# Kernel tuning notes

Hardware: AMD Instinct MI355X
Metric: run time of the kernel (lower is better)

The kernel has to match this reference:

```python
import jax, jax.numpy as jnp
import numpy as np

R = 32  # voxel resolution

def leaky(x):
    return jnp.where(x > 0, x, 0.1 * x)

def bn(x, gamma, beta, axes, eps=1e-4):
    mu = jnp.mean(x, axis=axes, keepdims=True)
    var = jnp.var(x, axis=axes, keepdims=True)
    shape = [1] * x.ndim
    shape[1] = x.shape[1]
    g = gamma.reshape(shape)
    b = beta.reshape(shape)
    return (x - mu) * jax.lax.rsqrt(var + eps) * g + b

def voxelize(features, coords, r):
    # features: (B, C, N), coords: (B, 3, N)
    B, C, N = features.shape
    mean = jnp.mean(coords, axis=2, keepdims=True)
    norm = (coords - mean + 1.0) / 2.0 * r
    norm = jnp.clip(norm, 0.0, r - 1.0)            # (B, 3, N) continuous voxel coords
    vox = jnp.round(norm).astype(jnp.int32)
    flat = (vox[:, 0] * r + vox[:, 1]) * r + vox[:, 2]      # (B, N)
    seg = (flat + jnp.arange(B, dtype=jnp.int32)[:, None] * (r ** 3)).reshape(-1)
    data = features.transpose(0, 2, 1).reshape(B * N, C)
    sums = jax.ops.segment_sum(data, seg, num_segments=B * r ** 3)
    cnt = jax.ops.segment_sum(jnp.ones((B * N,), data.dtype), seg, num_segments=B * r ** 3)
    avg = sums / jnp.maximum(cnt, 1.0)[:, None]
    grid = avg.reshape(B, r, r, r, C).transpose(0, 4, 1, 2, 3)  # (B, C, r, r, r)
    return grid, norm

def trilinear_devoxelize(grid, norm, r):
    # grid: (B, C, r, r, r), norm: (B, 3, N) in [0, r-1]
    B, C = grid.shape[:2]
    N = norm.shape[2]
    lo = jnp.floor(norm).astype(jnp.int32)
    frac = norm - lo.astype(norm.dtype)
    hi = jnp.minimum(lo + 1, r - 1)
    gf = grid.reshape(B, C, r ** 3)
    out = jnp.zeros((B, C, N), grid.dtype)
    for dx in (0, 1):
        for dy in (0, 1):
            for dz in (0, 1):
                ix = hi[:, 0] if dx else lo[:, 0]
                iy = hi[:, 1] if dy else lo[:, 1]
                iz = hi[:, 2] if dz else lo[:, 2]
                wx = frac[:, 0] if dx else 1.0 - frac[:, 0]
                wy = frac[:, 1] if dy else 1.0 - frac[:, 1]
                wz = frac[:, 2] if dz else 1.0 - frac[:, 2]
                idx = (ix * r + iy) * r + iz                    # (B, N)
                g = jnp.take_along_axis(gf, idx[:, None, :], axis=2)  # (B, C, N)
                out = out + g * (wx * wy * wz)[:, None, :]
    return out

def conv3d(x, w, b):
    y = jax.lax.conv_general_dilated(
        x, w, window_strides=(1, 1, 1), padding=[(1, 1)] * 3,
        dimension_numbers=('NCDHW', 'OIDHW', 'NCDHW'))
    return y + b[None, :, None, None, None]

def setup_inputs() -> dict:
    key = jax.random.key(0)
    ks = jax.random.split(key, 8)
    B, Cin, Cout, N = 8, 64, 64, 32768
    s1 = 1.0 / np.sqrt(Cin * 27)
    s2 = 1.0 / np.sqrt(Cout * 27)
    return {
        'features': jax.random.normal(ks[0], (B, Cin, N), jnp.float32),
        'coords': jax.random.normal(ks[1], (B, 3, N), jnp.float32),
        'conv1_w': jax.random.normal(ks[2], (Cout, Cin, 3, 3, 3), jnp.float32) * s1,
        'conv1_b': jnp.zeros((Cout,), jnp.float32),
        'bn1_g': jnp.ones((Cout,), jnp.float32),
        'bn1_b': jnp.zeros((Cout,), jnp.float32),
        'conv2_w': jax.random.normal(ks[3], (Cout, Cout, 3, 3, 3), jnp.float32) * s2,
        'conv2_b': jnp.zeros((Cout,), jnp.float32),
        'bn2_g': jnp.ones((Cout,), jnp.float32),
        'bn2_b': jnp.zeros((Cout,), jnp.float32),
        'mlp_w': jax.random.normal(ks[4], (Cout, Cin), jnp.float32) / np.sqrt(Cin),
        'mlp_b': jnp.zeros((Cout,), jnp.float32),
        'bnp_g': jnp.ones((Cout,), jnp.float32),
        'bnp_b': jnp.zeros((Cout,), jnp.float32),
    }

def reference(features, coords, conv1_w, conv1_b, bn1_g, bn1_b,
              conv2_w, conv2_b, bn2_g, bn2_b, mlp_w, mlp_b, bnp_g, bnp_b):
    grid, norm = voxelize(features, coords, R)
    v = leaky(bn(conv3d(grid, conv1_w, conv1_b), bn1_g, bn1_b, (0, 2, 3, 4)))
    v = leaky(bn(conv3d(v, conv2_w, conv2_b), bn2_g, bn2_b, (0, 2, 3, 4)))
    sampled = trilinear_devoxelize(v, norm, R)                 # (B, Cout, N)
    p = jnp.einsum('oi,bin->bon', mlp_w, features) + mlp_b[None, :, None]
    p = leaky(bn(p, bnp_g, bnp_b, (0, 2)))
    fused = sampled + p
    return fused, v
```

## Files before the change

kernel.cpp:

```cpp
#include <hip/hip_runtime.h>
#include <hip/hip_bf16.h>

#define BB 8
#define CC 64
#define NPTS 32768
#define RR 32
#define RV 32768
#define MTOT (BB*RV)
#define EPSV 1e-4f

#define OFF_BUFA 0u
#define OFF_BUFB 16777216u
#define OFF_WB1  25165824u
#define OFF_WB2  25221120u
#define OFF_ZG   25276416u
#define OFF_BASE 25276480u
#define OFF_AUX  25800768u
#define OFF_CELL 25801024u
#define OFF_CNT  26063168u
#define OFF_MEAN 26325312u
#define OFF_PART1 26325504u
#define OFF_PART2 26456576u
#define OFF_SCL1 26587648u
#define OFF_SFT1 26587712u
#define OFF_SCL2 26587776u
#define OFF_SFT2 26587840u
#define OFF_WM   26587904u
#define OFF_PARTP 26590208u
#define OFF_SCLP 27114496u
#define OFF_SFTP 27114560u
#define OFF_NORM 33554432u

typedef __attribute__((ext_vector_type(8))) __bf16 bf16x8;
typedef __attribute__((ext_vector_type(8))) unsigned short u16x8;
typedef __attribute__((ext_vector_type(4))) float f32x4;

__device__ __forceinline__ float b2f(ushort u) {
    union { unsigned u; float f; } x; x.u = ((unsigned)u) << 16; return x.f;
}
__device__ __forceinline__ ushort f2b(float f) {
    __hip_bfloat16 h = __float2bfloat16(f);
    return *reinterpret_cast<ushort*>(&h);
}

__global__ void k_coord_mean(const float* __restrict__ coords, float* __restrict__ mean) {
    int ba = blockIdx.x >> 3, ch = blockIdx.x & 7;
    const float* src = coords + (size_t)ba * NPTS + ch * 4096;
    float s = 0.f;
    for (int i = threadIdx.x; i < 4096; i += 256) s += src[i];
    __shared__ float red[256];
    red[threadIdx.x] = s; __syncthreads();
    for (int w = 128; w > 0; w >>= 1) {
        if (threadIdx.x < w) red[threadIdx.x] += red[threadIdx.x + w];
        __syncthreads();
    }
    if (threadIdx.x == 0) atomicAdd(&mean[ba], red[0]);
}

__global__ void k_cellid(const float* __restrict__ coords, const float* __restrict__ mean,
                         float* __restrict__ norm, int* __restrict__ cellid,
                         unsigned* __restrict__ cnt) {
    int idx = blockIdx.x * 256 + threadIdx.x;
    int b = idx >> 15, n = idx & (NPTS - 1);
    int flat = 0;
    #pragma unroll
    for (int a = 0; a < 3; ++a) {
        float c = coords[((size_t)(b * 3 + a)) * NPTS + n];
        float nm = (c - mean[b * 3 + a] * (1.0f / NPTS) + 1.0f) * (0.5f * RR);
        nm = fminf(fmaxf(nm, 0.0f), (float)(RR - 1));
        norm[((size_t)(b * 3 + a)) * NPTS + n] = nm;
        flat = flat * RR + (int)rintf(nm);
    }
    int cell = b * RV + flat;
    cellid[idx] = cell;
    atomicAdd(&cnt[cell], 1u);
}

__global__ void k_scan1(const unsigned* __restrict__ cnt, unsigned* __restrict__ base,
                        unsigned* __restrict__ aux) {
    int tid = threadIdx.x;
    int c0 = blockIdx.x * 1024 + tid * 4;
    unsigned v0 = cnt[c0], v1 = cnt[c0 + 1], v2 = cnt[c0 + 2], v3 = cnt[c0 + 3];
    unsigned tot = v0 + v1 + v2 + v3;
    __shared__ unsigned sc[256];
    sc[tid] = tot; __syncthreads();
    for (int off = 1; off < 256; off <<= 1) {
        unsigned t = (tid >= off) ? sc[tid - off] : 0u;
        __syncthreads();
        sc[tid] += t;
        __syncthreads();
    }
    unsigned excl = sc[tid] - tot;
    base[c0] = excl;
    base[c0 + 1] = excl + v0;
    base[c0 + 2] = excl + v0 + v1;
    base[c0 + 3] = excl + v0 + v1 + v2;
    if (tid == 255) aux[blockIdx.x] = sc[255];
}

__global__ void k_scan2(unsigned* __restrict__ aux) {
    int tid = threadIdx.x;
    unsigned own = aux[tid];
    __shared__ unsigned sc[256];
    sc[tid] = own; __syncthreads();
    for (int off = 1; off < 256; off <<= 1) {
        unsigned t = (tid >= off) ? sc[tid - off] : 0u;
        __syncthreads();
        sc[tid] += t;
        __syncthreads();
    }
    aux[tid] = sc[tid] - own;
}

__global__ void k_scan3(unsigned* __restrict__ base, const unsigned* __restrict__ aux) {
    int i = blockIdx.x * 256 + threadIdx.x;
    base[i] += aux[i >> 10];
}

__global__ __launch_bounds__(256) void k_scatfeat(
    const float* __restrict__ feats, const int* __restrict__ cellid,
    unsigned* __restrict__ base, ushort* __restrict__ fsort,
    const ushort* __restrict__ wmb, const float* __restrict__ mbias,
    ushort* __restrict__ pb, float* __restrict__ partp) {
    __shared__ float t[64 * 65];
    __shared__ unsigned spos[64];
    __shared__ float sf[512];
    int b = blockIdx.x >> 9;
    int n0 = (blockIdx.x & 511) * 64;
    int tid = threadIdx.x;
    #pragma unroll
    for (int k = 0; k < 16; ++k) {
        int idx = k * 256 + tid;
        int c = idx >> 6, nl = idx & 63;
        t[c * 65 + nl] = feats[((size_t)(b * 64 + c)) * NPTS + n0 + nl];
    }
    if (tid < 64) {
        int cell = cellid[(b << 15) + n0 + tid];
        spos[tid] = atomicAdd(&base[cell], 1u);
    }
    __syncthreads();
    #pragma unroll
    for (int it = 0; it < 2; ++it) {
        int pl = it * 32 + (tid >> 3);
        int j = tid & 7;
        unsigned pos = spos[pl];
        u16x8 v;
        #pragma unroll
        for (int k = 0; k < 8; ++k) v[k] = f2b(t[(j * 8 + k) * 65 + pl]);
        *reinterpret_cast<u16x8*>(fsort + (((size_t)pos) << 6) + j * 8) = v;
    }
    int w = tid >> 6, l = tid & 63;
    int nl = l & 15, kg = l >> 4;
    bf16x8 Af[2];
    #pragma unroll
    for (int ks = 0; ks < 2; ++ks) {
        union { u16x8 u; bf16x8 h; } cv;
        #pragma unroll
        for (int j = 0; j < 8; ++j)
            cv.u[j] = f2b(t[(ks * 32 + kg * 8 + j) * 65 + w * 16 + nl]);
        Af[ks] = cv.h;
    }
    f32x4 acc[4];
    #pragma unroll
    for (int cb = 0; cb < 4; ++cb) acc[cb] = (f32x4){0.f, 0.f, 0.f, 0.f};
    #pragma unroll
    for (int ks = 0; ks < 2; ++ks)
        #pragma unroll
        for (int cb = 0; cb < 4; ++cb) {
            bf16x8 Bf = *reinterpret_cast<const bf16x8*>(wmb + (cb * 16 + nl) * 64 + ks * 32 + kg * 8);
            acc[cb] = __builtin_amdgcn_mfma_f32_16x16x32_bf16(Af[ks], Bf, acc[cb], 0, 0, 0);
        }
    float ss[4] = {0.f, 0.f, 0.f, 0.f}, qq[4] = {0.f, 0.f, 0.f, 0.f};
    #pragma unroll
    for (int cb = 0; cb < 4; ++cb) {
        float bsv = mbias[cb * 16 + nl];
        #pragma unroll
        for (int r = 0; r < 4; ++r) {
            float yv = acc[cb][r] + bsv;
            int pt = w * 16 + kg * 4 + r;
            pb[(((size_t)((b << 15) + n0 + pt)) << 6) + cb * 16 + nl] = f2b(yv);
            ss[cb] += yv; qq[cb] += yv * yv;
        }
    }
    #pragma unroll
    for (int cb = 0; cb < 4; ++cb) {
        ss[cb] += __shfl_xor(ss[cb], 16); ss[cb] += __shfl_xor(ss[cb], 32);
        qq[cb] += __shfl_xor(qq[cb], 16); qq[cb] += __shfl_xor(qq[cb], 32);
    }
    if (l < 16) {
        #pragma unroll
        for (int cb = 0; cb < 4; ++cb) {
            sf[w * 128 + cb * 16 + nl] = ss[cb];
            sf[w * 128 + 64 + cb * 16 + nl] = qq[cb];
        }
    }
    __syncthreads();
    if (tid < 128)
        partp[(size_t)tid * 4096 + blockIdx.x] =
            sf[tid] + sf[128 + tid] + sf[256 + tid] + sf[384 + tid];
}

__global__ __launch_bounds__(256) void k_gather(
    const ushort* __restrict__ fsort, const unsigned* __restrict__ base,
    const unsigned* __restrict__ cnt, __hip_bfloat16* __restrict__ xb) {
    int cell = blockIdx.x * 4 + (threadIdx.x >> 6);
    int lane = threadIdx.x & 63;
    unsigned n = cnt[cell];
    unsigned start = base[cell] - n;
    const ushort* rows = fsort + (((size_t)start) << 6) + lane;
    float acc = 0.f;
    unsigned i = 0;
    for (; i + 8 <= n; i += 8) {
        float f0 = b2f(rows[((size_t)(i + 0)) << 6]);
        float f1 = b2f(rows[((size_t)(i + 1)) << 6]);
        float f2 = b2f(rows[((size_t)(i + 2)) << 6]);
        float f3 = b2f(rows[((size_t)(i + 3)) << 6]);
        float f4 = b2f(rows[((size_t)(i + 4)) << 6]);
        float f5 = b2f(rows[((size_t)(i + 5)) << 6]);
        float f6 = b2f(rows[((size_t)(i + 6)) << 6]);
        float f7 = b2f(rows[((size_t)(i + 7)) << 6]);
        acc += ((f0 + f1) + (f2 + f3)) + ((f4 + f5) + (f6 + f7));
    }
    for (; i < n; ++i) acc += b2f(rows[((size_t)i) << 6]);
    float inv = (n > 0) ? (1.0f / (float)n) : 0.f;
    xb[((size_t)cell << 6) + lane] = __float2bfloat16(acc * inv);
}

__global__ void k_wb(const float* __restrict__ w, __hip_bfloat16* __restrict__ wb) {
    int i = blockIdx.x * 256 + threadIdx.x;
    if (i >= CC * CC * 27) return;
    int tap = i % 27, t = i / 27;
    int ci = t & 63, co = t >> 6;
    wb[((size_t)(tap * 64 + co)) * 64 + ci] = __float2bfloat16(w[i]);
}

__global__ void k_wm(const float* __restrict__ w, ushort* __restrict__ wmb) {
    int i = blockIdx.x * 256 + threadIdx.x;
    if (i < 4096) wmb[i] = f2b(w[i]);
}

__global__ void k_act(const ushort* __restrict__ in, const float* __restrict__ scl,
                      const float* __restrict__ sft, ushort* __restrict__ out) {
    size_t i = ((size_t)blockIdx.x * 256 + threadIdx.x) << 3;
    u16x8 v = *reinterpret_cast<const u16x8*>(in + i);
    int c0 = (int)(i & 63);
    u16x8 o;
    #pragma unroll
    for (int j = 0; j < 8; ++j) {
        float f = fmaf(b2f(v[j]), scl[c0 + j], sft[c0 + j]);
        f = f > 0.f ? f : 0.1f * f;
        o[j] = f2b(f);
    }
    *reinterpret_cast<u16x8*>(out + i) = o;
}

__global__ __launch_bounds__(256, 1) void k_conv_mfma(
    const ushort* __restrict__ src, const ushort* __restrict__ wb,
    const float* __restrict__ bias, ushort* __restrict__ y,
    float* __restrict__ part, const ushort* __restrict__ zg) {
    __shared__ __align__(16) char sh[77824 + 49152];
    char* wsh = sh + 77824;
    int tid = threadIdx.x;
    int lane = tid & 63, wid = tid >> 6;
    int tile = ((blockIdx.x & 7) << 7) + (blockIdx.x >> 3);
    int twi = tile & 3, thi = (tile >> 2) & 3;
    int tdi = (tile >> 4) & 7, b = tile >> 7;
    int d0 = tdi * 4, h0 = thi * 8, w0 = twi * 8;

    auto stage_wgt = [&](int g) {
        const ushort* wgrp = wb + g * 12288;
        char* wdst0 = wsh + (g & 1) * 24576;
        #pragma unroll
        for (int i = 0; i < 6; ++i) {
            int c = (i * 4 + wid) * 64 + lane;
            int row = c >> 3, off = c & 7;
            const ushort* gsrc = wgrp + (((row << 3) + (off ^ (row & 7))) << 3);
            char* ldst = wdst0 + ((i * 4 + wid) << 10);
            __builtin_amdgcn_global_load_lds(
                (const __attribute__((address_space(1))) void*)gsrc,
                (__attribute__((address_space(3))) void*)ldst, 16, 0, 0);
        }
    };

    #pragma unroll
    for (int it = 0; it < 19; ++it) {
        int c = (it * 4 + wid) * 64 + lane;
        int row = c >> 3, off = c & 7;
        int dz = row / 100, rem = row - dz * 100;
        int hz = rem / 10, wz = rem - hz * 10;
        int gd = d0 - 1 + dz, gh = h0 - 1 + hz, gw = w0 - 1 + wz;
        int srcoff = off ^ (row & 7);
        const ushort* gsrc = ((unsigned)gd < 32u && (unsigned)gh < 32u && (unsigned)gw < 32u)
            ? src + ((((size_t)((b << 15) | (gd << 10) | (gh << 5) | gw)) << 6) + srcoff * 8)
            : zg;
        char* ldst = sh + ((it * 4 + wid) << 10);
        __builtin_amdgcn_global_load_lds(
            (const __attribute__((address_space(1))) void*)gsrc,
            (__attribute__((address_space(3))) void*)ldst, 16, 0, 0);
    }
    stage_wgt(0);

    int nl = lane & 15, kg = lane >> 4;
    int rbase = wid * 100 + (nl >> 3) * 10 + (nl & 7);
    int bswz = (nl & 7) << 4;

    f32x4 acc[4][4];
    #pragma unroll
    for (int mi = 0; mi < 4; ++mi)
        #pragma unroll
        for (int cb = 0; cb < 4; ++cb) acc[mi][cb] = (f32x4){0.f, 0.f, 0.f, 0.f};

    __syncthreads();

    #pragma unroll 1
    for (int g = 0; g < 9; ++g) {
        if (g < 8) stage_wgt(g + 1);
        const char* wlds = wsh + (g & 1) * 24576;
        int kd = g / 3, kh = g - kd * 3;
        int rr0 = rbase + kd * 100 + kh * 10;
        #pragma unroll
        for (int tl = 0; tl < 3; ++tl) {
            bf16x8 a[4][2];
            #pragma unroll
            for (int mi = 0; mi < 4; ++mi) {
                int r = rr0 + tl + mi * 20;
                int ba = ((r << 7) + (kg << 4)) ^ ((r & 7) << 4);
                a[mi][0] = *reinterpret_cast<const bf16x8*>(sh + ba);
                a[mi][1] = *reinterpret_cast<const bf16x8*>(sh + (ba ^ 64));
            }
            bf16x8 bf[4][2];
            #pragma unroll
            for (int cb = 0; cb < 4; ++cb) {
                int rowb = tl * 64 + cb * 16 + nl;
                int bb0 = ((rowb << 7) + (kg << 4)) ^ bswz;
                bf[cb][0] = *reinterpret_cast<const bf16x8*>(wlds + bb0);
                bf[cb][1] = *reinterpret_cast<const bf16x8*>(wlds + (bb0 ^ 64));
            }
            #pragma unroll
            for (int ks = 0; ks < 2; ++ks)
                #pragma unroll
                for (int mi = 0; mi < 4; ++mi)
                    #pragma unroll
                    for (int cb = 0; cb < 4; ++cb)
                        acc[mi][cb] = __builtin_amdgcn_mfma_f32_16x16x32_bf16(
                            a[mi][ks], bf[cb][ks], acc[mi][cb], 0, 0, 0);
        }
        __syncthreads();
    }

    int d = d0 + wid;
    float bs[4];
    #pragma unroll
    for (int cb = 0; cb < 4; ++cb) bs[cb] = bias[cb * 16 + nl];
    float ss[4] = {0.f, 0.f, 0.f, 0.f}, qq[4] = {0.f, 0.f, 0.f, 0.f};
    #pragma unroll
    for (int mi = 0; mi < 4; ++mi) {
        int h = h0 + mi * 2 + (kg >> 1);
        int w = w0 + (kg & 1) * 4;
        size_t vox = (size_t)((b << 15) | (d << 10) | (h << 5) | w);
        #pragma unroll
        for (int cb = 0; cb < 4; ++cb) {
            int co = cb * 16 + nl;
            #pragma unroll
            for (int r = 0; r < 4; ++r) {
                float yv = acc[mi][cb][r] + bs[cb];
                y[((vox + r) << 6) + co] = f2b(yv);
                ss[cb] += yv; qq[cb] += yv * yv;
            }
        }
    }
    #pragma unroll
    for (int cb = 0; cb < 4; ++cb) {
        ss[cb] += __shfl_xor(ss[cb], 16); ss[cb] += __shfl_xor(ss[cb], 32);
        qq[cb] += __shfl_xor(qq[cb], 16); qq[cb] += __shfl_xor(qq[cb], 32);
    }
    float* sf = (float*)sh;
    if (lane < 16) {
        #pragma unroll
        for (int cb = 0; cb < 4; ++cb) {
            sf[wid * 128 + cb * 16 + nl] = ss[cb];
            sf[wid * 128 + 64 + cb * 16 + nl] = qq[cb];
        }
    }
    __syncthreads();
    if (tid < 128) {
        float t = sf[tid] + sf[128 + tid] + sf[256 + tid] + sf[384 + tid];
        part[tid * 1024 + blockIdx.x] = t;
    }
}

__global__ void k_redbn(const float* __restrict__ part, const float* __restrict__ g,
                        const float* __restrict__ bb, float* __restrict__ scl,
                        float* __restrict__ sft, int cnt) {
    int c = blockIdx.x;
    float s = 0.f, q = 0.f;
    for (int i = threadIdx.x; i < cnt; i += 256) {
        s += part[(size_t)c * cnt + i];
        q += part[(size_t)(64 + c) * cnt + i];
    }
    __shared__ float rs[256], rq[256];
    rs[threadIdx.x] = s; rq[threadIdx.x] = q; __syncthreads();
    for (int w = 128; w > 0; w >>= 1) {
        if (threadIdx.x < w) { rs[threadIdx.x] += rs[threadIdx.x + w]; rq[threadIdx.x] += rq[threadIdx.x + w]; }
        __syncthreads();
    }
    if (threadIdx.x == 0) {
        float mu = rs[0] * (1.0f / MTOT);
        float var = rq[0] * (1.0f / MTOT) - mu * mu;
        float sc = g[c] * rsqrtf(var + EPSV);
        scl[c] = sc; sft[c] = bb[c] - mu * sc;
    }
}

__global__ void k_transpose(const ushort* __restrict__ in, const float* __restrict__ scl,
                            const float* __restrict__ sft, float* __restrict__ out) {
    __shared__ float t[64 * 65];
    size_t base = (size_t)blockIdx.x * 4096;
    int gv0 = blockIdx.x * 64;
    int b = gv0 >> 15;
    int vox0 = gv0 & 32767;
    int chl = threadIdx.x & 63;
    float sc = scl[chl], sf = sft[chl];
    #pragma unroll
    for (int k = 0; k < 16; ++k) {
        int idx = k * 256 + threadIdx.x;
        float v = fmaf(b2f(in[base + idx]), sc, sf);
        t[(idx >> 6) * 65 + (idx & 63)] = v > 0.f ? v : 0.1f * v;
    }
    __syncthreads();
    #pragma unroll
    for (int k = 0; k < 16; ++k) {
        int idx = k * 256 + threadIdx.x;
        int ch = idx >> 6, voxl = idx & 63;
        out[((size_t)(b * 64 + ch)) * RV + vox0 + voxl] = t[voxl * 65 + ch];
    }
}

__global__ __launch_bounds__(256) void k_final(
    float* __restrict__ out, const ushort* __restrict__ pbuf,
    const ushort* __restrict__ vraw, const float* __restrict__ norm,
    const float* __restrict__ scl, const float* __restrict__ sft,
    const float* __restrict__ sclp, const float* __restrict__ sftp) {
    __shared__ float smp[64 * 65];
    int b = blockIdx.x >> 9;
    int n0 = (blockIdx.x & 511) * 64;
    int wid = threadIdx.x >> 6, lane = threadIdx.x & 63;
    const ushort* gb = vraw + (((size_t)b) << 15) * CC;
    const float* nrm0 = norm + ((size_t)(b * 3)) * NPTS;
    float sc = scl[lane], sf = sft[lane];
    float scp = sclp[lane], sfp = sftp[lane];

    #pragma unroll 2
    for (int i = 0; i < 16; ++i) {
        int pl = wid * 16 + i;
        int n = n0 + pl;
        float v0 = nrm0[n];
        float v1 = nrm0[NPTS + n];
        float v2 = nrm0[2 * NPTS + n];
        int lx = (int)floorf(v0), ly = (int)floorf(v1), lz = (int)floorf(v2);
        float fx = v0 - (float)lx, fy = v1 - (float)ly, fz = v2 - (float)lz;
        int hx = min(lx + 1, 31), hy = min(ly + 1, 31), hz = min(lz + 1, 31);
        float gx = 1.f - fx, gy = 1.f - fy, gz = 1.f - fz;

        int i000 = ((lx * 32 + ly) * 32 + lz) << 6;
        int i001 = ((lx * 32 + ly) * 32 + hz) << 6;
        int i010 = ((lx * 32 + hy) * 32 + lz) << 6;
        int i011 = ((lx * 32 + hy) * 32 + hz) << 6;
        int i100 = ((hx * 32 + ly) * 32 + lz) << 6;
        int i101 = ((hx * 32 + ly) * 32 + hz) << 6;
        int i110 = ((hx * 32 + hy) * 32 + lz) << 6;
        int i111 = ((hx * 32 + hy) * 32 + hz) << 6;

        float w000 = gx * gy * gz, w001 = gx * gy * fz;
        float w010 = gx * fy * gz, w011 = gx * fy * fz;
        float w100 = fx * gy * gz, w101 = fx * gy * fz;
        float w110 = fx * fy * gz, w111 = fx * fy * fz;

        float r0 = fmaf(b2f(gb[i000 + lane]), sc, sf); r0 = r0 > 0.f ? r0 : 0.1f * r0;
        float r1 = fmaf(b2f(gb[i001 + lane]), sc, sf); r1 = r1 > 0.f ? r1 : 0.1f * r1;
        float r2 = fmaf(b2f(gb[i010 + lane]), sc, sf); r2 = r2 > 0.f ? r2 : 0.1f * r2;
        float r3 = fmaf(b2f(gb[i011 + lane]), sc, sf); r3 = r3 > 0.f ? r3 : 0.1f * r3;
        float r4 = fmaf(b2f(gb[i100 + lane]), sc, sf); r4 = r4 > 0.f ? r4 : 0.1f * r4;
        float r5 = fmaf(b2f(gb[i101 + lane]), sc, sf); r5 = r5 > 0.f ? r5 : 0.1f * r5;
        float r6 = fmaf(b2f(gb[i110 + lane]), sc, sf); r6 = r6 > 0.f ? r6 : 0.1f * r6;
        float r7 = fmaf(b2f(gb[i111 + lane]), sc, sf); r7 = r7 > 0.f ? r7 : 0.1f * r7;

        float s = r0 * w000 + r1 * w001 + r2 * w010 + r3 * w011
                + r4 * w100 + r5 * w101 + r6 * w110 + r7 * w111;

        float pv = fmaf(b2f(pbuf[(((size_t)((b << 15) + n)) << 6) + lane]), scp, sfp);
        pv = pv > 0.f ? pv : 0.1f * pv;
        smp[pl * 65 + lane] = s + pv;
    }
    __syncthreads();

    #pragma unroll 4
    for (int i = 0; i < 16; ++i) {
        int co = i * 4 + wid;
        out[((size_t)(b * 64 + co)) * NPTS + n0 + lane] = smp[lane * 65 + co];
    }
}

extern "C" void kernel_launch(void* const* d_in, const int* in_sizes, int n_in,
                              void* d_out, int out_size, void* d_ws, size_t ws_size,
                              hipStream_t stream) {
    const float* features = (const float*)d_in[0];
    const float* coords   = (const float*)d_in[1];
    const float* conv1_w  = (const float*)d_in[2];
    const float* conv1_b  = (const float*)d_in[3];
    const float* bn1_g    = (const float*)d_in[4];
    const float* bn1_b    = (const float*)d_in[5];
    const float* conv2_w  = (const float*)d_in[6];
    const float* conv2_b  = (const float*)d_in[7];
    const float* bn2_g    = (const float*)d_in[8];
    const float* bn2_b    = (const float*)d_in[9];
    const float* mlp_w    = (const float*)d_in[10];
    const float* mlp_b    = (const float*)d_in[11];
    const float* bnp_g    = (const float*)d_in[12];
    const float* bnp_b    = (const float*)d_in[13];

    float* ws    = (float*)d_ws;
    ushort* fsort  = (ushort*)(ws + OFF_BUFA);
    ushort* y2b    = (ushort*)(ws + OFF_BUFA);
    ushort* x2b    = (ushort*)(ws + OFF_BUFA) + (size_t)16777216;
    __hip_bfloat16* xb  = (__hip_bfloat16*)(ws + OFF_BUFB);
    __hip_bfloat16* wb1 = (__hip_bfloat16*)(ws + OFF_WB1);
    __hip_bfloat16* wb2 = (__hip_bfloat16*)(ws + OFF_WB2);
    ushort* zg   = (ushort*)(ws + OFF_ZG);
    unsigned* base    = (unsigned*)(ws + OFF_BASE);
    unsigned* aux     = (unsigned*)(ws + OFF_AUX);
    int* cellid       = (int*)(ws + OFF_CELL);
    unsigned* cnt     = (unsigned*)(ws + OFF_CNT);
    float* mean  = ws + OFF_MEAN;
    float* part1 = ws + OFF_PART1;
    float* part2 = ws + OFF_PART2;
    float* scl1  = ws + OFF_SCL1;
    float* sft1  = ws + OFF_SFT1;
    float* scl2  = ws + OFF_SCL2;
    float* sft2  = ws + OFF_SFT2;
    ushort* wmb  = (ushort*)(ws + OFF_WM);
    float* partp = ws + OFF_PARTP;
    float* sclp  = ws + OFF_SCLP;
    float* sftp  = ws + OFF_SFTP;
    float* nrm   = ws + OFF_NORM;

    float* outF  = (float*)d_out;
    float* outV  = (float*)d_out + (size_t)16777216;
    ushort* y1b  = (ushort*)outV;
    ushort* pbuf = (ushort*)(outV + (size_t)8388608);

    hipMemsetAsync(cnt, 0, 262144 * 4, stream);
    hipMemsetAsync(zg, 0, 256, stream);
    hipMemsetAsync(mean, 0, 24 * 4, stream);

    k_coord_mean<<<192, 256, 0, stream>>>(coords, mean);
    k_cellid<<<1024, 256, 0, stream>>>(coords, mean, nrm, cellid, cnt);
    k_scan1<<<256, 256, 0, stream>>>(cnt, base, aux);
    k_scan2<<<1, 256, 0, stream>>>(aux);
    k_scan3<<<1024, 256, 0, stream>>>(base, aux);

    k_wb<<<432, 256, 0, stream>>>(conv1_w, wb1);
    k_wb<<<432, 256, 0, stream>>>(conv2_w, wb2);
    k_wm<<<16, 256, 0, stream>>>(mlp_w, wmb);

    k_scatfeat<<<4096, 256, 0, stream>>>(features, cellid, base, fsort,
                                         wmb, mlp_b, pbuf, partp);
    k_redbn<<<64, 256, 0, stream>>>(partp, bnp_g, bnp_b, sclp, sftp, 4096);
    k_gather<<<65536, 256, 0, stream>>>(fsort, base, cnt, xb);

    k_conv_mfma<<<1024, 256, 0, stream>>>((const ushort*)xb, (const ushort*)wb1, conv1_b,
                                          y1b, part1, zg);
    k_redbn<<<64, 256, 0, stream>>>(part1, bn1_g, bn1_b, scl1, sft1, 1024);

    k_act<<<8192, 256, 0, stream>>>(y1b, scl1, sft1, x2b);

    k_conv_mfma<<<1024, 256, 0, stream>>>(x2b, (const ushort*)wb2, conv2_b,
                                          y2b, part2, zg);
    k_redbn<<<64, 256, 0, stream>>>(part2, bn2_g, bn2_b, scl2, sft2, 1024);

    k_final<<<4096, 256, 0, stream>>>(outF, pbuf, y2b, nrm, scl2, sft2, sclp, sftp);

    k_transpose<<<4096, 256, 0, stream>>>(y2b, scl2, sft2, outV);
}
```

Baseline: 396.0 us.

## Enlarge conv tile to 8x8x8 voxels and stage weights per kernel tap

The 3D conv kernel now has each block compute an 8x8x8 output tile instead of 4x8x8, with each wave producing two depth slices (8 M-subtiles). The weight staging changes from per-(kd,kh) groups of 3 taps to single taps, double-buffered in a smaller LDS region so that a larger input halo (10x10x10) fits. This halves the block count and raises A-fragment reuse per weight load, cutting redundant halo loads. In exchange it adds more accumulator registers, 27 barrier iterations instead of 9, and an extra sync before the reduction scratch is reused.

```diff
diff --git a/kernel.cpp b/kernel.cpp
--- a/kernel.cpp
+++ b/kernel.cpp
@@ -258,24 +258,25 @@
     const ushort* __restrict__ src, const ushort* __restrict__ wb,
     const float* __restrict__ bias, ushort* __restrict__ y,
     float* __restrict__ part, const ushort* __restrict__ zg) {
-    __shared__ __align__(16) char sh[77824 + 49152];
-    char* wsh = sh + 77824;
+    __shared__ __align__(16) char sh[128000 + 16384];
+    char* wsh = sh + 128000;
     int tid = threadIdx.x;
     int lane = tid & 63, wid = tid >> 6;
-    int tile = ((blockIdx.x & 7) << 7) + (blockIdx.x >> 3);
+    int tile = ((blockIdx.x & 7) << 6) | (blockIdx.x >> 3);
     int twi = tile & 3, thi = (tile >> 2) & 3;
-    int tdi = (tile >> 4) & 7, b = tile >> 7;
-    int d0 = tdi * 4, h0 = thi * 8, w0 = twi * 8;
-
-    auto stage_wgt = [&](int g) {
-        const ushort* wgrp = wb + g * 12288;
-        char* wdst0 = wsh + (g & 1) * 24576;
-        #pragma unroll
-        for (int i = 0; i < 6; ++i) {
-            int c = (i * 4 + wid) * 64 + lane;
+    int tdi = (tile >> 4) & 3, b = tile >> 6;
+    int d0 = tdi * 8, h0 = thi * 8, w0 = twi * 8;
+
+    auto stage_wgt = [&](int t) {
+        const ushort* wgrp = wb + t * 4096;
+        char* wdst0 = wsh + (t & 1) * 8192;
+        #pragma unroll
+        for (int i = 0; i < 2; ++i) {
+            int idx = i * 4 + wid;
+            int c = idx * 64 + lane;
             int row = c >> 3, off = c & 7;
             const ushort* gsrc = wgrp + (((row << 3) + (off ^ (row & 7))) << 3);
-            char* ldst = wdst0 + ((i * 4 + wid) << 10);
+            char* ldst = wdst0 + (idx << 10);
             __builtin_amdgcn_global_load_lds(
                 (const __attribute__((address_space(1))) void*)gsrc,
                 (__attribute__((address_space(3))) void*)ldst, 16, 0, 0);
@@ -283,79 +284,79 @@
     };
 
     #pragma unroll
-    for (int it = 0; it < 19; ++it) {
-        int c = (it * 4 + wid) * 64 + lane;
-        int row = c >> 3, off = c & 7;
-        int dz = row / 100, rem = row - dz * 100;
-        int hz = rem / 10, wz = rem - hz * 10;
-        int gd = d0 - 1 + dz, gh = h0 - 1 + hz, gw = w0 - 1 + wz;
-        int srcoff = off ^ (row & 7);
-        const ushort* gsrc = ((unsigned)gd < 32u && (unsigned)gh < 32u && (unsigned)gw < 32u)
-            ? src + ((((size_t)((b << 15) | (gd << 10) | (gh << 5) | gw)) << 6) + srcoff * 8)
-            : zg;
-        char* ldst = sh + ((it * 4 + wid) << 10);
-        __builtin_amdgcn_global_load_lds(
-            (const __attribute__((address_space(1))) void*)gsrc,
-            (__attribute__((address_space(3))) void*)ldst, 16, 0, 0);
+    for (int it = 0; it < 32; ++it) {
+        int idx = it * 4 + wid;
+        if (idx < 125) {
+            int c = idx * 64 + lane;
+            int row = c >> 3, off = c & 7;
+            int dz = row / 100, rem = row - dz * 100;
+            int hz = rem / 10, wz = rem - hz * 10;
+            int gd = d0 - 1 + dz, gh = h0 - 1 + hz, gw = w0 - 1 + wz;
+            int srcoff = off ^ (row & 7);
+            const ushort* gsrc = ((unsigned)gd < 32u && (unsigned)gh < 32u && (unsigned)gw < 32u)
+                ? src + ((((size_t)((b << 15) | (gd << 10) | (gh << 5) | gw)) << 6) + srcoff * 8)
+                : zg;
+            char* ldst = sh + (idx << 10);
+            __builtin_amdgcn_global_load_lds(
+                (const __attribute__((address_space(1))) void*)gsrc,
+                (__attribute__((address_space(3))) void*)ldst, 16, 0, 0);
+        }
     }
     stage_wgt(0);
 
     int nl = lane & 15, kg = lane >> 4;
-    int rbase = wid * 100 + (nl >> 3) * 10 + (nl & 7);
-    int bswz = (nl & 7) << 4;
-
-    f32x4 acc[4][4];
-    #pragma unroll
-    for (int mi = 0; mi < 4; ++mi)
+    int rbase = (wid * 2) * 100 + (nl >> 3) * 10 + (nl & 7);
+    int bbase[4];
+    #pragma unroll
+    for (int cb = 0; cb < 4; ++cb)
+        bbase[cb] = (((cb * 16 + nl) << 7) + (kg << 4)) ^ ((nl & 7) << 4);
+
+    f32x4 acc[8][4];
+    #pragma unroll
+    for (int mi = 0; mi < 8; ++mi)
         #pragma unroll
         for (int cb = 0; cb < 4; ++cb) acc[mi][cb] = (f32x4){0.f, 0.f, 0.f, 0.f};
 
     __syncthreads();
 
     #pragma unroll 1
-    for (int g = 0; g < 9; ++g) {
-        if (g < 8) stage_wgt(g + 1);
-        const char* wlds = wsh + (g & 1) * 24576;
-        int kd = g / 3, kh = g - kd * 3;
-        int rr0 = rbase + kd * 100 + kh * 10;
-        #pragma unroll
-        for (int tl = 0; tl < 3; ++tl) {
-            bf16x8 a[4][2];
+    for (int t = 0; t < 27; ++t) {
+        if (t < 26) stage_wgt(t + 1);
+        const char* wlds = wsh + (t & 1) * 8192;
+        int kd = t / 9, rm = t - kd * 9;
+        int kh = rm / 3, kw = rm - kh * 3;
+        int rt = rbase + kd * 100 + kh * 10 + kw;
+        #pragma unroll
+        for (int ks = 0; ks < 2; ++ks) {
+            bf16x8 a[8];
             #pragma unroll
-            for (int mi = 0; mi < 4; ++mi) {
-                int r = rr0 + tl + mi * 20;
-                int ba = ((r << 7) + (kg << 4)) ^ ((r & 7) << 4);
-                a[mi][0] = *reinterpret_cast<const bf16x8*>(sh + ba);
-                a[mi][1] = *reinterpret_cast<const bf16x8*>(sh + (ba ^ 64));
+            for (int mi = 0; mi < 8; ++mi) {
+                int r = rt + (mi >> 2) * 100 + (mi & 3) * 20;
+                int ba = ((((r << 7) + (kg << 4)) ^ ((r & 7) << 4))) ^ (ks << 6);
+                a[mi] = *reinterpret_cast<const bf16x8*>(sh + ba);
             }
-            bf16x8 bf[4][2];
+            bf16x8 bf[4];
             #pragma unroll
-            for (int cb = 0; cb < 4; ++cb) {
-                int rowb = tl * 64 + cb * 16 + nl;
-                int bb0 = ((rowb << 7) + (kg << 4)) ^ bswz;
-                bf[cb][0] = *reinterpret_cast<const bf16x8*>(wlds + bb0);
-                bf[cb][1] = *reinterpret_cast<const bf16x8*>(wlds + (bb0 ^ 64));
-            }
+            for (int cb = 0; cb < 4; ++cb)
+                bf[cb] = *reinterpret_cast<const bf16x8*>(wlds + (bbase[cb] ^ (ks << 6)));
             #pragma unroll
-            for (int ks = 0; ks < 2; ++ks)
+            for (int mi = 0; mi < 8; ++mi)
                 #pragma unroll
-                for (int mi = 0; mi < 4; ++mi)
-                    #pragma unroll
-                    for (int cb = 0; cb < 4; ++cb)
-                        acc[mi][cb] = __builtin_amdgcn_mfma_f32_16x16x32_bf16(
-                            a[mi][ks], bf[cb][ks], acc[mi][cb], 0, 0, 0);
-        }
-        __syncthreads();
-    }
-
-    int d = d0 + wid;
+                for (int cb = 0; cb < 4; ++cb)
+                    acc[mi][cb] = __builtin_amdgcn_mfma_f32_16x16x32_bf16(
+                        a[mi], bf[cb], acc[mi][cb], 0, 0, 0);
+        }
+        __syncthreads();
+    }
+
     float bs[4];
     #pragma unroll
     for (int cb = 0; cb < 4; ++cb) bs[cb] = bias[cb * 16 + nl];
     float ss[4] = {0.f, 0.f, 0.f, 0.f}, qq[4] = {0.f, 0.f, 0.f, 0.f};
     #pragma unroll
-    for (int mi = 0; mi < 4; ++mi) {
-        int h = h0 + mi * 2 + (kg >> 1);
+    for (int mi = 0; mi < 8; ++mi) {
+        int d = d0 + wid * 2 + (mi >> 2);
+        int h = h0 + (mi & 3) * 2 + (kg >> 1);
         int w = w0 + (kg & 1) * 4;
         size_t vox = (size_t)((b << 15) | (d << 10) | (h << 5) | w);
         #pragma unroll
@@ -375,6 +376,7 @@
         qq[cb] += __shfl_xor(qq[cb], 16); qq[cb] += __shfl_xor(qq[cb], 32);
     }
     float* sf = (float*)sh;
+    __syncthreads();
     if (lane < 16) {
         #pragma unroll
         for (int cb = 0; cb < 4; ++cb) {
@@ -385,7 +387,7 @@
     __syncthreads();
     if (tid < 128) {
         float t = sf[tid] + sf[128 + tid] + sf[256 + tid] + sf[384 + tid];
-        part[tid * 1024 + blockIdx.x] = t;
+        part[tid * 512 + blockIdx.x] = t;
     }
 }
 
@@ -568,15 +570,15 @@
     k_redbn<<<64, 256, 0, stream>>>(partp, bnp_g, bnp_b, sclp, sftp, 4096);
     k_gather<<<65536, 256, 0, stream>>>(fsort, base, cnt, xb);
 
-    k_conv_mfma<<<1024, 256, 0, stream>>>((const ushort*)xb, (const ushort*)wb1, conv1_b,
-                                          y1b, part1, zg);
-    k_redbn<<<64, 256, 0, stream>>>(part1, bn1_g, bn1_b, scl1, sft1, 1024);
+    k_conv_mfma<<<512, 256, 0, stream>>>((const ushort*)xb, (const ushort*)wb1, conv1_b,
+                                         y1b, part1, zg);
+    k_redbn<<<64, 256, 0, stream>>>(part1, bn1_g, bn1_b, scl1, sft1, 512);
 
     k_act<<<8192, 256, 0, stream>>>(y1b, scl1, sft1, x2b);
 
-    k_conv_mfma<<<1024, 256, 0, stream>>>(x2b, (const ushort*)wb2, conv2_b,
-                                          y2b, part2, zg);
-    k_redbn<<<64, 256, 0, stream>>>(part2, bn2_g, bn2_b, scl2, sft2, 1024);
+    k_conv_mfma<<<512, 256, 0, stream>>>(x2b, (const ushort*)wb2, conv2_b,
+                                         y2b, part2, zg);
+    k_redbn<<<64, 256, 0, stream>>>(part2, bn2_g, bn2_b, scl2, sft2, 512);
 
     k_final<<<4096, 256, 0, stream>>>(outF, pbuf, y2b, nrm, scl2, sft2, sclp, sftp);
 
```

New measurement: 398.9 us. About the same (+0.7%).
